# Performance work log

Hardware: AMD Instinct MI355X
Metric: run time of the kernel (lower is better)

The kernel has to match this reference:

```python
import jax, jax.numpy as jnp
import numpy as np

EPS = 1e-4

def _conv(x, W):
    # x: [B,H,W,Cin], W: [3,3,Cin,Cout] -> SAME submanifold-style dense conv
    return jax.lax.conv_general_dilated(x, W, (1, 1), 'SAME',
                                        dimension_numbers=('NHWC', 'HWIO', 'NHWC'))

def _bn_relu(x, m, g, b):
    # BatchNormReLU over active sites only (scn semantics)
    mm = m[..., None]
    n = jnp.maximum(mm.sum(), 1.0)
    mean = (x * mm).sum((0, 1, 2)) / n
    var = (((x - mean) ** 2) * mm).sum((0, 1, 2)) / n
    y = (x - mean) * jax.lax.rsqrt(var + EPS) * g + b
    return jnp.maximum(y, 0.0) * mm

def _maxpool(x, m):
    # scn.MaxPooling(2, 3, 2): 3x3 window, stride 2, VALID; output active if any input active
    neg = jnp.where(m[..., None] > 0, x, -1e30)
    p = jax.lax.reduce_window(neg, -1e30, jax.lax.max, (1, 3, 3, 1), (1, 2, 2, 1), 'VALID')
    m2 = jax.lax.reduce_window(m, 0.0, jax.lax.max, (1, 3, 3), (1, 2, 2), 'VALID')
    return jnp.where(m2[..., None] > 0, p, 0.0), m2


def setup_inputs() -> dict:
    key = jax.random.key(0)
    ks = jax.random.split(key, 16)
    B, H, W = 2048, 23, 31
    x = jax.random.normal(ks[0], (B, H, W, 2), dtype=jnp.float32)
    mask = jax.random.randint(ks[1], (B, H, W), 0, 2, dtype=jnp.int32)
    def w(k, shape, s=0.05):
        return jax.random.normal(k, shape, dtype=jnp.float32) * s
    params = {
        'x': x, 'mask': mask,
        'W1': w(ks[2], (3, 3, 2, 16)),   'g1': jnp.ones(16),  'b1': jnp.zeros(16),
        'W2': w(ks[3], (3, 3, 16, 32)),  'g2': jnp.ones(32),  'b2': jnp.zeros(32),
        'W3': w(ks[4], (3, 3, 32, 64)),  'g3': jnp.ones(64),  'b3': jnp.zeros(64),
        'W4': w(ks[5], (3, 3, 64, 128)), 'g4': jnp.ones(128), 'b4': jnp.zeros(128),
        'Wl': w(ks[6], (3, 3, 128, 4 * 256)), 'bl': jnp.zeros(4 * 256),
        'lw1': w(ks[7], (8960, 1024), 0.02), 'lb1': jnp.zeros(1024),
        'lw2': w(ks[8], (1024, 5 * 7 * 12), 0.02), 'lb2': jnp.zeros(5 * 7 * 12),
    }
    return params


def reference(x, mask, W1, g1, b1, W2, g2, b2, W3, g3, b3, W4, g4, b4,
              Wl, bl, lw1, lb1, lw2, lb2):
    m = mask.astype(x.dtype)
    xm = x * m[..., None]
    h = _bn_relu(_conv(xm, W1) * m[..., None], m, g1, b1)
    h = _bn_relu(_conv(h, W2) * m[..., None], m, g2, b2)
    h, m = _maxpool(h, m)                          # [B,11,15,32]
    h = _bn_relu(_conv(h, W3) * m[..., None], m, g3, b3)
    h = _bn_relu(_conv(h, W4) * m[..., None], m, g4, b4)
    h, m = _maxpool(h, m)                          # [B,5,7,128]
    # sparse ConvLSTM, single step, zero initial hidden/cell state
    gates = (_conv(h, Wl) + bl) * m[..., None]     # [B,5,7,1024]
    i, f, o, g_ = jnp.split(gates, 4, axis=-1)
    c = jax.nn.sigmoid(i) * jnp.tanh(g_)
    hh = jax.nn.sigmoid(o) * jnp.tanh(c) * m[..., None]  # [B,5,7,256]
    # SparseToDense gives [B,C,H,W]; flatten in (C,H,W) order like torch .view
    flat = jnp.transpose(hh, (0, 3, 1, 2)).reshape(hh.shape[0], -1)  # [B,8960]
    y = jnp.maximum(flat @ lw1 + lb1, 0.0)
    y = y @ lw2 + lb2
    return y.reshape(-1, 5, 7, 12)
```

## Files before the change

kernel.cpp:

```cpp
#include <hip/hip_runtime.h>
#include <hip/hip_bf16.h>
#include <math.h>

using bf16 = __hip_bfloat16;

typedef short s8v __attribute__((ext_vector_type(8)));
typedef float f4v __attribute__((ext_vector_type(4)));

static constexpr int  BB  = 2048;
static constexpr int  IH  = 23, IW = 31;
static constexpr int  PH  = 11, PW = 15;
static constexpr int  QH  = 5,  QW = 7;
static constexpr long NSITE1 = (long)BB * IH * IW;
static constexpr long NSITE2 = (long)BB * PH * PW;
static constexpr long NSITE3 = (long)BB * QH * QW;

static constexpr long OFF_S1 = 0,   OFF_Q1 = 64;
static constexpr long OFF_S2 = 128, OFF_Q2 = 192;
static constexpr long OFF_S3 = 256, OFF_Q3 = 320;
static constexpr long OFF_S4 = 384, OFF_Q4 = 512;
static constexpr long OFF_N1 = 640, OFF_N2 = 641;
static constexpr long OFF_SC1 = 704,  OFF_SH1 = 768;
static constexpr long OFF_SC2 = 832,  OFF_SH2 = 896;
static constexpr long OFF_SC3 = 960,  OFF_SH3 = 1024;
static constexpr long OFF_SC4 = 1088, OFF_SH4 = 1216;
static constexpr long OFF_M0 = 2048;
static constexpr long OFF_M1 = OFF_M0 + NSITE1;
static constexpr long OFF_M2 = OFF_M1 + NSITE2;
static constexpr long OFF_BF = 1871872;
static constexpr long SZ_A   = 43253760L;
static constexpr long WB2_A  = 25000000L;
static constexpr long WB3_B  = 22000000L;
static constexpr long WB4_B  = 22100000L;
static constexpr long WBL_A  = 20000000L;
static constexpr long WFC1_B = 23000000L;
static constexpr long WFC2_B = 33000000L;

__device__ __forceinline__ float b2f(bf16 v) { return __bfloat162float(v); }
__device__ __forceinline__ bf16  f2b(float v) { return __float2bfloat16(v); }
__device__ __forceinline__ float sigmoidf_(float x) {
    return __builtin_amdgcn_rcpf(1.f + __expf(-x));
}
__device__ __forceinline__ float tanhf_(float x) {
    float xc = fminf(fmaxf(x, -15.f), 15.f);
    float t = __expf(-2.f * xc);
    return (1.f - t) * __builtin_amdgcn_rcpf(1.f + t);
}

__device__ __forceinline__ void ld8(const bf16* p, float* f) {
    union { uint4 u; unsigned short s[8]; } cv;
    cv.u = *(const uint4*)p;
#pragma unroll
    for (int i = 0; i < 8; i++) f[i] = __uint_as_float(((unsigned int)cv.s[i]) << 16);
}
__device__ __forceinline__ void st8(bf16* p, const float* f) {
    union { uint4 u; bf16 h[8]; } cv;
#pragma unroll
    for (int i = 0; i < 8; i++) cv.h[i] = f2b(f[i]);
    *(uint4*)p = cv.u;
}

__global__ void cvt_w_k(const float* __restrict__ W, bf16* __restrict__ wb,
                        int CIN, int CINP, int COUT, int total) {
    int idx = blockIdx.x * 256 + threadIdx.x;
    if (idx >= total) return;
    int ci  = idx % CINP;
    int t2  = idx / CINP;
    int co  = t2 % COUT;
    int tap = t2 / COUT;
    wb[idx] = (ci < CIN) ? f2b(W[((long)(tap * CIN + ci)) * COUT + co]) : f2b(0.f);
}

__global__ void cvt_wl3_k(const float* __restrict__ Wl, bf16* __restrict__ wbl3) {
    int idx = blockIdx.x * 256 + threadIdx.x;
    if (idx >= 884736) return;
    int kidx = idx & 31;
    int n    = (idx >> 5) % 768;
    int kk   = (idx >> 5) / 768 % 4;
    int tap  = idx / (32 * 768 * 4);
    int g = n >> 8, c = n & 255;
    int col = (g == 0) ? c : (g == 1 ? 512 + c : 768 + c);
    int cin = kk * 32 + kidx;
    wbl3[idx] = f2b(Wl[((long)(tap * 128 + cin)) * 1024 + col]);
}

__global__ void cvt_fc1T8_k(const float* __restrict__ lw1, bf16* __restrict__ wfc1) {
    int t = blockIdx.x * 256 + threadIdx.x;
    if (t >= 1146880) return;
    int j   = t & 1023;
    int k8g = t >> 10;
    int hw  = k8g >> 5;
    int c8  = k8g & 31;
    float f[8];
#pragma unroll
    for (int c7 = 0; c7 < 8; c7++)
        f[c7] = lw1[((long)((c8 * 8 + c7) * 35 + hw)) * 1024 + j];
    st8(wfc1 + (long)t * 8, f);
}

__global__ void cvt_fc2T8_k(const float* __restrict__ lw2, bf16* __restrict__ whi,
                            bf16* __restrict__ wlo) {
    int t = blockIdx.x * 256 + threadIdx.x;
    if (t >= 57344) return;
    int n  = t % 448;
    int k8 = t / 448;
    union { uint4 u; bf16 h8[8]; } h, l;
#pragma unroll
    for (int ki = 0; ki < 8; ki++) {
        float v = (n < 420) ? lw2[(long)(k8 * 8 + ki) * 420 + n] : 0.f;
        bf16 hb = f2b(v);
        h.h8[ki] = hb;
        l.h8[ki] = f2b(v - b2f(hb));
    }
    *(uint4*)(whi + (long)t * 8) = h.u;
    *(uint4*)(wlo + (long)t * 8) = l.u;
}

__global__ void prep_k(const float* __restrict__ x, const int* __restrict__ mask,
                       float* __restrict__ m0, bf16* __restrict__ xm) {
    long idx = (long)blockIdx.x * 256 + threadIdx.x;
    if (idx >= NSITE1) return;
    float m = (mask[idx] != 0) ? 1.f : 0.f;
    m0[idx] = m;
    xm[idx * 2 + 0] = f2b(x[idx * 2 + 0] * m);
    xm[idx * 2 + 1] = f2b(x[idx * 2 + 1] * m);
}

__global__ void conv1_k(const bf16* __restrict__ xm, const float* __restrict__ Wt,
                        const float* __restrict__ m0, bf16* __restrict__ out) {
    const int H = IH, W = IW;
    long site = (long)blockIdx.x * 256 + threadIdx.x;
    if (site >= NSITE1) return;
    float acc[16];
#pragma unroll
    for (int i = 0; i < 16; i++) acc[i] = 0.f;
    float mk = m0[site];
    if (mk > 0.f) {
        int w = (int)(site % W); int h = (int)((site / W) % H);
        for (int tap = 0; tap < 9; tap++) {
            int dh = tap / 3 - 1, dw = tap % 3 - 1;
            int nh = h + dh, nw = w + dw;
            if (nh < 0 || nh >= H || nw < 0 || nw >= W) continue;
            long ns = site + (long)dh * W + dw;
            float i0 = b2f(xm[ns * 2 + 0]), i1 = b2f(xm[ns * 2 + 1]);
            const float* wp = Wt + tap * 32;
#pragma unroll
            for (int co = 0; co < 16; co++) acc[co] += i0 * wp[co] + i1 * wp[16 + co];
        }
    }
    st8(out + site * 16, acc);
    st8(out + site * 16 + 8, acc + 8);
}

template<int CIN, int CINP, int COUT, int KK, int MT_W, int NT_W, int H, int W, bool ZPAD>
__global__ void conv_mfma(const bf16* __restrict__ in, const bf16* __restrict__ wb,
                          const float* __restrict__ mask, bf16* __restrict__ out) {
    constexpr int NT   = COUT / 16;
    constexpr int NWN  = NT / NT_W;
    constexpr int HALO = W + 1;
    constexpr int REG  = 64 + 2 * HALO;
    constexpr int SE   = CIN + 8;
    constexpr int CHPS = CIN / 8;
    __shared__ bf16 smem[(REG + 1) * SE];

    const int tid = threadIdx.x;
    const int wv = tid >> 6;
    const int L  = tid & 63;
    const int q  = (L >> 4);
    const int lm = L & 15;
    const int wn = wv % NWN;
    const int wm = wv / NWN;
    const int mt0 = wm * MT_W;
    const long base = (long)blockIdx.x * 64;
    const long nsites = (long)gridDim.x * 64;

    for (int c = tid; c < REG * CHPS; c += 256) {
        int s = c / CHPS;
        int o = c % CHPS;
        long gs = base - HALO + s;
        uint4 v = {0u, 0u, 0u, 0u};
        if (gs >= 0 && gs < nsites) v = *(const uint4*)(in + gs * CIN + o * 8);
        *(uint4*)(smem + s * SE + o * 8) = v;
    }
    if (ZPAD) {
        uint4 z = {0u, 0u, 0u, 0u};
        for (int s = tid; s < REG; s += 256)
            *(uint4*)(smem + s * SE + CIN) = z;
        if (tid == 0)
            *(uint4*)(smem + REG * SE) = z;
    }
    __syncthreads();

    int hh[MT_W], ww[MT_W];
#pragma unroll
    for (int i = 0; i < MT_W; i++) {
        long s = base + (mt0 + i) * 16 + lm;
        ww[i] = (int)(s % W);
        hh[i] = (int)((s / W) % H);
    }
    const int lbase = mt0 * 16 + lm + HALO;

    f4v acc[MT_W][NT_W];
#pragma unroll
    for (int i = 0; i < MT_W; i++)
#pragma unroll
        for (int j = 0; j < NT_W; j++) acc[i][j] = (f4v){0.f, 0.f, 0.f, 0.f};

    for (int tap = 0; tap < 9; tap++) {
        const int dh = tap / 3 - 1, dw = tap % 3 - 1;
        const int dlo = dh * W + dw;
#pragma unroll
        for (int kk = 0; kk < KK; kk++) {
            s8v a[MT_W];
#pragma unroll
            for (int i = 0; i < MT_W; i++) {
                int nh = hh[i] + dh, nw = ww[i] + dw;
                bool ok = (nh >= 0) & (nh < H) & (nw < W) & (nw >= 0);
                s8v t = *(const s8v*)(smem + (lbase + i * 16 + dlo) * SE + kk * 32 + q * 8);
                a[i] = ok ? t : (s8v){0, 0, 0, 0, 0, 0, 0, 0};
            }
#pragma unroll
            for (int j = 0; j < NT_W; j++) {
                int co = (wn * NT_W + j) * 16 + lm;
                s8v b = *(const s8v*)(wb + ((long)(tap * COUT + co)) * CINP + kk * 32 + q * 8);
#pragma unroll
                for (int i = 0; i < MT_W; i++)
                    acc[i][j] = __builtin_amdgcn_mfma_f32_16x16x32_bf16(a[i], b, acc[i][j], 0, 0, 0);
            }
        }
    }
#pragma unroll
    for (int i = 0; i < MT_W; i++) {
#pragma unroll
        for (int r = 0; r < 4; r++) {
            long so = base + (mt0 + i) * 16 + q * 4 + r;
            float mk = mask[so];
#pragma unroll
            for (int j = 0; j < NT_W; j++) {
                int co = (wn * NT_W + j) * 16 + lm;
                out[so * COUT + co] = f2b(mk > 0.f ? acc[i][j][r] : 0.f);
            }
        }
    }
}

template<int C>
__global__ void bn_stats(const bf16* __restrict__ v, const float* __restrict__ mask,
                         float* __restrict__ sum, float* __restrict__ sumsq,
                         float* __restrict__ count, long nsites) {
    __shared__ float s_sum[C], s_ss[C];
    __shared__ float s_cnt;
    int tid = threadIdx.x;
    if (tid < C) { s_sum[tid] = 0.f; s_ss[tid] = 0.f; }
    if (tid == 0) s_cnt = 0.f;
    __syncthreads();
    const long total8 = nsites * C / 8;
    const long stride = (long)gridDim.x * 256;
    const int c0 = (int)((((long)blockIdx.x * 256 + tid) * 8) % C);
    float ls[8], lss[8];
#pragma unroll
    for (int i = 0; i < 8; i++) { ls[i] = 0.f; lss[i] = 0.f; }
    float lc = 0.f;
    for (long e8 = (long)blockIdx.x * 256 + tid; e8 < total8; e8 += stride) {
        long e0 = e8 * 8;
        float f[8];
        ld8(v + e0, f);
#pragma unroll
        for (int i = 0; i < 8; i++) { ls[i] += f[i]; lss[i] += f[i] * f[i]; }
        if (count != nullptr && c0 == 0) lc += (mask[e0 / C] > 0.f) ? 1.f : 0.f;
    }
#pragma unroll
    for (int i = 0; i < 8; i++) {
        atomicAdd(&s_sum[c0 + i], ls[i]);
        atomicAdd(&s_ss[c0 + i], lss[i]);
    }
    if (count != nullptr && c0 == 0) atomicAdd(&s_cnt, lc);
    __syncthreads();
    if (tid < C) { atomicAdd(&sum[tid], s_sum[tid]); atomicAdd(&sumsq[tid], s_ss[tid]); }
    if (count != nullptr && tid == 0) atomicAdd(count, s_cnt);
}

template<int C>
__global__ void bn_param(const float* __restrict__ sum, const float* __restrict__ ss,
                         const float* __restrict__ count,
                         const float* __restrict__ g, const float* __restrict__ b,
                         float* __restrict__ scale, float* __restrict__ shift) {
    int c = threadIdx.x;
    if (c >= C) return;
    float n = fmaxf(count[0], 1.f);
    float mean = sum[c] / n;
    float var  = ss[c] / n - mean * mean;
    float sc = (1.f / sqrtf(var + 1e-4f)) * g[c];
    scale[c] = sc;
    shift[c] = b[c] - mean * sc;
}

template<int C>
__global__ void bn_apply(bf16* __restrict__ v, const float* __restrict__ mask,
                         const float* __restrict__ scale, const float* __restrict__ shift,
                         long nsites) {
    long i8 = (long)blockIdx.x * 256 + threadIdx.x;
    if (i8 >= nsites * C / 8) return;
    long e0 = i8 * 8;
    int c0 = (int)(e0 % C);
    long site = e0 / C;
    float mk = mask[site];
    float f[8], o[8];
    ld8(v + e0, f);
#pragma unroll
    for (int i = 0; i < 8; i++)
        o[i] = (mk > 0.f) ? fmaxf(f[i] * scale[c0 + i] + shift[c0 + i], 0.f) : 0.f;
    st8(v + e0, o);
}

template<int C>
__global__ void maxpool_bn(const bf16* __restrict__ in, const float* __restrict__ min_,
                           const float* __restrict__ scale, const float* __restrict__ shift,
                           bf16* __restrict__ out, float* __restrict__ mout,
                           int B, int H, int W, int OH, int OW) {
    long i8 = (long)blockIdx.x * 256 + threadIdx.x;
    long total8 = (long)B * OH * OW * C / 8;
    if (i8 >= total8) return;
    long e0 = i8 * 8;
    int c0 = (int)(e0 % C);
    long osite = e0 / C;
    int ow = (int)(osite % OW); long t2 = osite / OW; int oh = (int)(t2 % OH); long b = t2 / OH;
    float sc[8], sh[8];
#pragma unroll
    for (int i = 0; i < 8; i++) { sc[i] = scale[c0 + i]; sh[i] = shift[c0 + i]; }
    float mm = 0.f, p[8];
#pragma unroll
    for (int i = 0; i < 8; i++) p[i] = -1e30f;
    for (int kh = 0; kh < 3; kh++)
    for (int kw = 0; kw < 3; kw++) {
        int h = oh * 2 + kh, w = ow * 2 + kw;
        long is = ((long)b * H + h) * W + w;
        float mv = min_[is];
        if (mv > 0.f) {
            mm = 1.f;
            float f[8];
            ld8(in + is * C + c0, f);
#pragma unroll
            for (int i = 0; i < 8; i++) p[i] = fmaxf(p[i], f[i] * sc[i] + sh[i]);
        }
    }
    float o[8];
#pragma unroll
    for (int i = 0; i < 8; i++) o[i] = (mm > 0.f) ? fmaxf(p[i], 0.f) : 0.f;
    st8(out + e0, o);
    if (c0 == 0) mout[osite] = mm;
}

__global__ void maxpool_p2t(const bf16* __restrict__ c4, const float* __restrict__ m1,
                            const float* __restrict__ scale, const float* __restrict__ shift,
                            bf16* __restrict__ p2T8, float* __restrict__ m2h) {
    int t = blockIdx.x * 256 + threadIdx.x;
    if (t >= 1146880) return;
    int b  = t & 2047;
    int q2 = t >> 11;
    int hw = q2 % 35;
    int k8 = q2 / 35;
    int oh = hw / QW, ow = hw % QW;
    int c0 = k8 * 8;
    float sc[8], sh[8];
#pragma unroll
    for (int i = 0; i < 8; i++) { sc[i] = scale[c0 + i]; sh[i] = shift[c0 + i]; }
    float mm = 0.f, p[8];
#pragma unroll
    for (int i = 0; i < 8; i++) p[i] = -1e30f;
    for (int kh = 0; kh < 3; kh++)
    for (int kw = 0; kw < 3; kw++) {
        int h = oh * 2 + kh, w = ow * 2 + kw;
        long is = ((long)b * PH + h) * PW + w;
        float mv = m1[is];
        if (mv > 0.f) {
            mm = 1.f;
            float f[8];
            ld8(c4 + is * 128 + c0, f);
#pragma unroll
            for (int i = 0; i < 8; i++) p[i] = fmaxf(p[i], f[i] * sc[i] + sh[i]);
        }
    }
    float o[8];
#pragma unroll
    for (int i = 0; i < 8; i++) o[i] = (mm > 0.f) ? fmaxf(p[i], 0.f) : 0.f;
    st8(p2T8 + (long)t * 8, o);
    if (k8 == 0) m2h[hw * 2048 + b] = mm;
}

__global__ void __launch_bounds__(256, 3)
gates_mfma(const bf16* __restrict__ p2T8, const bf16* __restrict__ wbl3,
           const float* __restrict__ bl, const float* __restrict__ m2h,
           bf16* __restrict__ goutT8) {
    __shared__ bf16 abuf[16 * 64 * 8];
    __shared__ bf16 sm[64][136];
    const int d = blockIdx.x;
    const int bi = (d & 7) * 280 + (d >> 3);
    const int half = bi & 1;
    const int g2 = bi >> 1;
    const int hw = g2 >> 5;
    const int b0 = (g2 & 31) * 64;
    const int h = hw / QW, w = hw % QW;
    const int tid = threadIdx.x;
    const int wv = tid >> 6;
    const int L  = tid & 63;
    const int q  = L >> 4;
    const int lm = L & 15;

    f4v acc[4][2][3];
#pragma unroll
    for (int i = 0; i < 4; i++)
#pragma unroll
        for (int j = 0; j < 2; j++)
#pragma unroll
            for (int g = 0; g < 3; g++) acc[i][j][g] = (f4v){0.f, 0.f, 0.f, 0.f};

    for (int tap = 0; tap < 9; tap++) {
        const int dh = tap / 3 - 1, dw = tap % 3 - 1;
        const int nh = h + dh, nw = w + dw;
        if (nh < 0 || nh >= QH || nw < 0 || nw >= QW) continue;
        const int hwn = hw + dh * QW + dw;

        __syncthreads();
        for (int c = tid; c < 1024; c += 256) {
            int kq = c >> 6;
            int bb = c & 63;
            uint4 v = *(const uint4*)(p2T8 + (((long)(kq * 35 + hwn)) * 2048 + b0 + bb) * 8);
            *(uint4*)(abuf + (long)c * 8) = v;
        }
        __syncthreads();

#pragma unroll
        for (int kk = 0; kk < 4; kk++) {
            s8v a[4];
#pragma unroll
            for (int i = 0; i < 4; i++)
                a[i] = *(const s8v*)(abuf + (((kk * 4 + q) * 64) + i * 16 + lm) * 8);
            const bf16* slab = wbl3 + ((long)(tap * 4 + kk)) * 768 * 32 + (long)q * 8;
#pragma unroll
            for (int j = 0; j < 2; j++) {
                int cc = half * 8 + wv * 2 + j;
#pragma unroll
                for (int g = 0; g < 3; g++) {
                    int n = g * 256 + cc * 16 + lm;
                    s8v b = *(const s8v*)(slab + (long)n * 32);
#pragma unroll
                    for (int i = 0; i < 4; i++)
                        acc[i][j][g] = __builtin_amdgcn_mfma_f32_16x16x32_bf16(a[i], b, acc[i][j][g], 0, 0, 0);
                }
            }
        }
    }
#pragma unroll
    for (int j = 0; j < 2; j++) {
        int cc = half * 8 + wv * 2 + j;
        int c = cc * 16 + lm;
        int cl = (wv * 2 + j) * 16 + lm;
        float bi_ = bl[c], bo_ = bl[512 + c], bg_ = bl[768 + c];
#pragma unroll
        for (int i = 0; i < 4; i++) {
#pragma unroll
            for (int r = 0; r < 4; r++) {
                int b_in = i * 16 + q * 4 + r;
                float m = m2h[hw * 2048 + b0 + b_in];
                float val = 0.f;
                if (m > 0.f) {
                    float iv = acc[i][j][0][r] + bi_;
                    float ov = acc[i][j][1][r] + bo_;
                    float gv = acc[i][j][2][r] + bg_;
                    float ct = sigmoidf_(iv) * tanhf_(gv);
                    val = sigmoidf_(ov) * tanhf_(ct);
                }
                sm[b_in][cl] = f2b(val);
            }
        }
    }
    __syncthreads();
#pragma unroll
    for (int k = 0; k < 4; k++) {
        int e = k * 256 + tid;
        int c8l = e >> 6, b_in = e & 63;
        union { uint4 u; bf16 h8[8]; } v;
#pragma unroll
        for (int i = 0; i < 8; i++) v.h8[i] = sm[b_in][c8l * 8 + i];
        long dst = ((long)(hw * 32 + half * 16 + c8l)) * 2048 + b0 + b_in;
        *(uint4*)(goutT8 + dst * 8) = v.u;
    }
}

__global__ void fc1_mfma(const bf16* __restrict__ AT8, const bf16* __restrict__ WT8,
                         const float* __restrict__ lb1, bf16* __restrict__ y1) {
    const int tid = threadIdx.x;
    const int wv = tid >> 6;
    const int L  = tid & 63;
    const int q  = L >> 4, lm = L & 15;
    const int wm = wv >> 1, wn = wv & 1;
    const int bm = blockIdx.x & 31;
    const int bn = blockIdx.x >> 5;
    const int m0 = bm * 64 + wm * 32;
    const int n0 = bn * 64 + wn * 32;

    f4v acc[2][2];
#pragma unroll
    for (int i = 0; i < 2; i++)
#pragma unroll
        for (int j = 0; j < 2; j++) acc[i][j] = (f4v){0.f, 0.f, 0.f, 0.f};

#pragma unroll 2
    for (int k8 = 0; k8 < 1120; k8 += 4) {
        long ar = ((long)(k8 + q)) * 2048;
        long br = ((long)(k8 + q)) * 1024;
        s8v a0 = *(const s8v*)(AT8 + (ar + m0 + lm) * 8);
        s8v a1 = *(const s8v*)(AT8 + (ar + m0 + 16 + lm) * 8);
        s8v b0 = *(const s8v*)(WT8 + (br + n0 + lm) * 8);
        s8v b1 = *(const s8v*)(WT8 + (br + n0 + 16 + lm) * 8);
        acc[0][0] = __builtin_amdgcn_mfma_f32_16x16x32_bf16(a0, b0, acc[0][0], 0, 0, 0);
        acc[0][1] = __builtin_amdgcn_mfma_f32_16x16x32_bf16(a0, b1, acc[0][1], 0, 0, 0);
        acc[1][0] = __builtin_amdgcn_mfma_f32_16x16x32_bf16(a1, b0, acc[1][0], 0, 0, 0);
        acc[1][1] = __builtin_amdgcn_mfma_f32_16x16x32_bf16(a1, b1, acc[1][1], 0, 0, 0);
    }
#pragma unroll
    for (int i = 0; i < 2; i++) {
#pragma unroll
        for (int j = 0; j < 2; j++) {
            int nn = n0 + j * 16 + lm;
            float bias = lb1[nn];
#pragma unroll
            for (int r = 0; r < 4; r++) {
                int mm = m0 + i * 16 + q * 4 + r;
                y1[(long)mm * 1024 + nn] = f2b(fmaxf(acc[i][j][r] + bias, 0.f));
            }
        }
    }
}

__global__ void fc2_mfma(const bf16* __restrict__ y1, const bf16* __restrict__ whi,
                         const bf16* __restrict__ wlo, const float* __restrict__ lb2,
                         float* __restrict__ out) {
    const int tid = threadIdx.x;
    const int wv = tid >> 6;
    const int L  = tid & 63;
    const int q  = L >> 4, lm = L & 15;
    const int wm = wv >> 1, wn = wv & 1;
    const int bm = blockIdx.x % 32;
    const int bn = blockIdx.x / 32;
    const int m0 = bm * 64 + wm * 32;
    const int n0 = bn * 64 + wn * 32;

    f4v acc[2][2];
#pragma unroll
    for (int i = 0; i < 2; i++)
#pragma unroll
        for (int j = 0; j < 2; j++) acc[i][j] = (f4v){0.f, 0.f, 0.f, 0.f};

#pragma unroll 2
    for (int k8 = 0; k8 < 128; k8 += 4) {
        const bf16* arow = y1 + (long)(k8 + q) * 8;
        long br = ((long)(k8 + q)) * 448;
        s8v a0 = *(const s8v*)(arow + (long)(m0 + lm) * 1024);
        s8v a1 = *(const s8v*)(arow + (long)(m0 + 16 + lm) * 1024);
        s8v h0 = *(const s8v*)(whi + (br + n0 + lm) * 8);
        s8v h1 = *(const s8v*)(whi + (br + n0 + 16 + lm) * 8);
        s8v l0 = *(const s8v*)(wlo + (br + n0 + lm) * 8);
        s8v l1 = *(const s8v*)(wlo + (br + n0 + 16 + lm) * 8);
        acc[0][0] = __builtin_amdgcn_mfma_f32_16x16x32_bf16(a0, h0, acc[0][0], 0, 0, 0);
        acc[0][1] = __builtin_amdgcn_mfma_f32_16x16x32_bf16(a0, h1, acc[0][1], 0, 0, 0);
        acc[1][0] = __builtin_amdgcn_mfma_f32_16x16x32_bf16(a1, h0, acc[1][0], 0, 0, 0);
        acc[1][1] = __builtin_amdgcn_mfma_f32_16x16x32_bf16(a1, h1, acc[1][1], 0, 0, 0);
        acc[0][0] = __builtin_amdgcn_mfma_f32_16x16x32_bf16(a0, l0, acc[0][0], 0, 0, 0);
        acc[0][1] = __builtin_amdgcn_mfma_f32_16x16x32_bf16(a0, l1, acc[0][1], 0, 0, 0);
        acc[1][0] = __builtin_amdgcn_mfma_f32_16x16x32_bf16(a1, l0, acc[1][0], 0, 0, 0);
        acc[1][1] = __builtin_amdgcn_mfma_f32_16x16x32_bf16(a1, l1, acc[1][1], 0, 0, 0);
    }
#pragma unroll
    for (int j = 0; j < 2; j++) {
        int nn = n0 + j * 16 + lm;
        if (nn >= 420) continue;
        float bias = lb2[nn];
#pragma unroll
        for (int i = 0; i < 2; i++) {
#pragma unroll
            for (int r = 0; r < 4; r++) {
                int mm = m0 + i * 16 + q * 4 + r;
                out[(long)mm * 420 + nn] = acc[i][j][r] + bias;
            }
        }
    }
}

extern "C" void kernel_launch(void* const* d_in, const int* in_sizes, int n_in,
                              void* d_out, int out_size, void* d_ws, size_t ws_size,
                              hipStream_t stream) {
    const float* x    = (const float*)d_in[0];
    const int*   mask = (const int*)d_in[1];
    const float* W1 = (const float*)d_in[2];
    const float* g1 = (const float*)d_in[3];
    const float* b1 = (const float*)d_in[4];
    const float* W2 = (const float*)d_in[5];
    const float* g2 = (const float*)d_in[6];
    const float* b2 = (const float*)d_in[7];
    const float* W3 = (const float*)d_in[8];
    const float* g3 = (const float*)d_in[9];
    const float* b3 = (const float*)d_in[10];
    const float* W4 = (const float*)d_in[11];
    const float* g4 = (const float*)d_in[12];
    const float* b4 = (const float*)d_in[13];
    const float* Wl = (const float*)d_in[14];
    const float* bl = (const float*)d_in[15];
    const float* lw1 = (const float*)d_in[16];
    const float* lb1 = (const float*)d_in[17];
    const float* lw2 = (const float*)d_in[18];
    const float* lb2 = (const float*)d_in[19];
    float* out = (float*)d_out;

    float* ws = (float*)d_ws;
    float* m0 = ws + OFF_M0;
    float* m1 = ws + OFF_M1;
    float* m2h = ws + OFF_M2;
    bf16* bufA = (bf16*)(ws + OFF_BF);
    bf16* bufB = bufA + SZ_A;

    bf16* c1     = bufA;
    bf16* xm     = bufB;
    bf16* c2     = bufB;
    bf16* p1     = bufA;
    bf16* c3     = bufB;
    bf16* c4     = bufA;
    bf16* p2T8   = bufB;
    bf16* goutT8 = bufA;
    bf16* y1     = bufB;
    bf16* wb2    = bufA + WB2_A;
    bf16* wb3    = bufB + WB3_B;
    bf16* wb4    = bufB + WB4_B;
    bf16* wbl3   = bufA + WBL_A;
    bf16* wfc1   = bufB + WFC1_B;
    bf16* wfc2h  = bufB + WFC2_B;
    bf16* wfc2l  = wfc2h + 458752;

    hipMemsetAsync(ws, 0, 4096, stream);

    prep_k<<<(int)((NSITE1 + 255) / 256), 256, 0, stream>>>(x, mask, m0, xm);
    cvt_w_k<<<(9216 + 255) / 256, 256, 0, stream>>>(W2, wb2, 16, 32, 32, 9216);

    conv1_k<<<(int)((NSITE1 + 255) / 256), 256, 0, stream>>>(xm, W1, m0, c1);
    bn_stats<16><<<1280, 256, 0, stream>>>(c1, m0, ws + OFF_S1, ws + OFF_Q1, ws + OFF_N1, NSITE1);
    bn_param<16><<<1, 16, 0, stream>>>(ws + OFF_S1, ws + OFF_Q1, ws + OFF_N1, g1, b1, ws + OFF_SC1, ws + OFF_SH1);
    bn_apply<16><<<(int)(NSITE1 * 16 / 8 / 256), 256, 0, stream>>>(c1, m0, ws + OFF_SC1, ws + OFF_SH1, NSITE1);

    conv_mfma<16, 32, 32, 1, 2, 1, IH, IW, true><<<(int)(NSITE1 / 64), 256, 0, stream>>>(c1, wb2, m0, c2);
    bn_stats<32><<<1280, 256, 0, stream>>>(c2, m0, ws + OFF_S2, ws + OFF_Q2, nullptr, NSITE1);
    bn_param<32><<<1, 32, 0, stream>>>(ws + OFF_S2, ws + OFF_Q2, ws + OFF_N1, g2, b2, ws + OFF_SC2, ws + OFF_SH2);

    maxpool_bn<32><<<(int)(NSITE2 * 32 / 8 / 256), 256, 0, stream>>>(c2, m0, ws + OFF_SC2, ws + OFF_SH2,
                                                                     p1, m1, BB, IH, IW, PH, PW);

    cvt_w_k<<<(18432 + 255) / 256, 256, 0, stream>>>(W3, wb3, 32, 32, 64, 18432);
    cvt_w_k<<<(73728 + 255) / 256, 256, 0, stream>>>(W4, wb4, 64, 64, 128, 73728);
    cvt_fc1T8_k<<<(1146880 + 255) / 256, 256, 0, stream>>>(lw1, wfc1);
    cvt_fc2T8_k<<<(57344 + 255) / 256, 256, 0, stream>>>(lw2, wfc2h, wfc2l);

    conv_mfma<32, 32, 64, 1, 4, 1, PH, PW, false><<<(int)(NSITE2 / 64), 256, 0, stream>>>(p1, wb3, m1, c3);
    bn_stats<64><<<1280, 256, 0, stream>>>(c3, m1, ws + OFF_S3, ws + OFF_Q3, ws + OFF_N2, NSITE2);
    bn_param<64><<<1, 64, 0, stream>>>(ws + OFF_S3, ws + OFF_Q3, ws + OFF_N2, g3, b3, ws + OFF_SC3, ws + OFF_SH3);
    bn_apply<64><<<(int)(NSITE2 * 64 / 8 / 256), 256, 0, stream>>>(c3, m1, ws + OFF_SC3, ws + OFF_SH3, NSITE2);

    conv_mfma<64, 64, 128, 2, 4, 2, PH, PW, false><<<(int)(NSITE2 / 64), 256, 0, stream>>>(c3, wb4, m1, c4);
    bn_stats<128><<<1280, 256, 0, stream>>>(c4, m1, ws + OFF_S4, ws + OFF_Q4, nullptr, NSITE2);
    bn_param<128><<<1, 128, 0, stream>>>(ws + OFF_S4, ws + OFF_Q4, ws + OFF_N2, g4, b4, ws + OFF_SC4, ws + OFF_SH4);

    maxpool_p2t<<<(1146880 + 255) / 256, 256, 0, stream>>>(c4, m1, ws + OFF_SC4, ws + OFF_SH4, p2T8, m2h);

    cvt_wl3_k<<<(884736 + 255) / 256, 256, 0, stream>>>(Wl, wbl3);

    gates_mfma<<<2240, 256, 0, stream>>>(p2T8, wbl3, bl, m2h, goutT8);

    fc1_mfma<<<512, 256, 0, stream>>>(goutT8, wfc1, lb1, y1);

    fc2_mfma<<<224, 256, 0, stream>>>(y1, wfc2h, wfc2l, lb2, out);
}
```

Before: 1.040 ms.

## Double-buffer activation tiles in gates kernel and drop block index swizzle

The gates MFMA kernel now keeps two LDS activation buffers and loads the next valid tap's activations into registers while the MFMAs for the current tap run, then writes them to the other buffer. This removes one barrier per tap and hides global load latency behind compute. It also drops the blockIdx remapping that grouped blocks across spatial positions, which changes the L2 access locality for weights and activations. LDS use grows by 16 KB per block, which may reduce occupancy, and the prefetched values raise register pressure.

Result: no change. 1.039 ms (-0.2%).

```diff
diff --git a/kernel.cpp b/kernel.cpp
--- a/kernel.cpp
+++ b/kernel.cpp
@@ -392,10 +392,9 @@
 gates_mfma(const bf16* __restrict__ p2T8, const bf16* __restrict__ wbl3,
            const float* __restrict__ bl, const float* __restrict__ m2h,
            bf16* __restrict__ goutT8) {
-    __shared__ bf16 abuf[16 * 64 * 8];
+    __shared__ bf16 abuf[2][16 * 64 * 8];
     __shared__ bf16 sm[64][136];
-    const int d = blockIdx.x;
-    const int bi = (d & 7) * 280 + (d >> 3);
+    const int bi = blockIdx.x;
     const int half = bi & 1;
     const int g2 = bi >> 1;
     const int hw = g2 >> 5;
@@ -415,28 +414,52 @@
 #pragma unroll
             for (int g = 0; g < 3; g++) acc[i][j][g] = (f4v){0.f, 0.f, 0.f, 0.f};
 
-    for (int tap = 0; tap < 9; tap++) {
-        const int dh = tap / 3 - 1, dw = tap % 3 - 1;
-        const int nh = h + dh, nw = w + dw;
-        if (nh < 0 || nh >= QH || nw < 0 || nw >= QW) continue;
-        const int hwn = hw + dh * QW + dw;
-
-        __syncthreads();
-        for (int c = tid; c < 1024; c += 256) {
-            int kq = c >> 6;
-            int bb = c & 63;
+    auto tap_hwn = [&](int tap) { return hw + (tap / 3 - 1) * QW + (tap % 3 - 1); };
+    auto tap_ok  = [&](int tap) {
+        int nh = h + tap / 3 - 1, nw = w + tap % 3 - 1;
+        return (nh >= 0) & (nh < QH) & (nw >= 0) & (nw < QW);
+    };
+
+    int ctap = 0;
+    while (!tap_ok(ctap)) ctap++;
+
+    {
+        int hwn = tap_hwn(ctap);
+#pragma unroll
+        for (int r = 0; r < 4; r++) {
+            int c = tid + r * 256;
+            int kq = c >> 6, bb = c & 63;
             uint4 v = *(const uint4*)(p2T8 + (((long)(kq * 35 + hwn)) * 2048 + b0 + bb) * 8);
-            *(uint4*)(abuf + (long)c * 8) = v;
-        }
-        __syncthreads();
-
+            *(uint4*)(&abuf[0][0] + (long)c * 8) = v;
+        }
+    }
+    __syncthreads();
+
+    int cur = 0;
+    while (ctap >= 0) {
+        int ntap = -1;
+        for (int t2 = ctap + 1; t2 < 9; t2++)
+            if (tap_ok(t2)) { ntap = t2; break; }
+
+        uint4 pref[4];
+        if (ntap >= 0) {
+            int hwn = tap_hwn(ntap);
+#pragma unroll
+            for (int r = 0; r < 4; r++) {
+                int c = tid + r * 256;
+                int kq = c >> 6, bb = c & 63;
+                pref[r] = *(const uint4*)(p2T8 + (((long)(kq * 35 + hwn)) * 2048 + b0 + bb) * 8);
+            }
+        }
+
+        const bf16* ab = &abuf[cur][0];
 #pragma unroll
         for (int kk = 0; kk < 4; kk++) {
             s8v a[4];
 #pragma unroll
             for (int i = 0; i < 4; i++)
-                a[i] = *(const s8v*)(abuf + (((kk * 4 + q) * 64) + i * 16 + lm) * 8);
-            const bf16* slab = wbl3 + ((long)(tap * 4 + kk)) * 768 * 32 + (long)q * 8;
+                a[i] = *(const s8v*)(ab + (((kk * 4 + q) * 64) + i * 16 + lm) * 8);
+            const bf16* slab = wbl3 + ((long)(ctap * 4 + kk)) * 768 * 32 + (long)q * 8;
 #pragma unroll
             for (int j = 0; j < 2; j++) {
                 int cc = half * 8 + wv * 2 + j;
@@ -450,7 +473,20 @@
                 }
             }
         }
-    }
+
+        if (ntap >= 0) {
+            bf16* wbuf = &abuf[cur ^ 1][0];
+#pragma unroll
+            for (int r = 0; r < 4; r++) {
+                int c = tid + r * 256;
+                *(uint4*)(wbuf + (long)c * 8) = pref[r];
+            }
+        }
+        __syncthreads();
+        cur ^= 1;
+        ctap = ntap;
+    }
+
 #pragma unroll
     for (int j = 0; j < 2; j++) {
         int cc = half * 8 + wv * 2 + j;
```
